# Kernel optimization log

Measured on AMD Instinct MI355X. Metric: run time of the kernel, lower is better.

Reference implementation:

```python
import jax, jax.numpy as jnp
import numpy as np

B, N_IN, N_OUT = 4096, 64, 64
M = N_IN * N_OUT


def setup_inputs() -> dict:
    key = jax.random.key(0)
    k1, k2, k3, k4 = jax.random.split(key, 4)
    I = jax.random.normal(k1, (B, N_IN, 4, 4), dtype=jnp.float32)
    # params: (rand - 0.5) * 1, matching torch init
    aW = (jax.random.uniform(k2, (M, 1, 1), dtype=jnp.float32) - 0.5)
    uW = (jax.random.uniform(k3, (M, 1, 3), dtype=jnp.float32) - 0.5)
    tW = (jax.random.uniform(k4, (M, 1, 3), dtype=jnp.float32) - 0.5)
    return {"I": I, "aW": aW, "uW": uW, "tW": tW}


def _build_WM(aW, uW, tW, n_in, n_out):
    m = aW.shape[0]
    a = aW.reshape(m, 1, 1)                       # angle per transform
    u = jax.nn.sigmoid(uW.reshape(m, 3))
    u = u / jnp.linalg.norm(u, axis=1, keepdims=True)  # unit axis
    ux, uy, uz = u[:, 0], u[:, 1], u[:, 2]
    z = jnp.zeros_like(ux)
    # skew-symmetric cross-product matrix K
    K = jnp.stack([z, -uz, uy,
                   uz, z, -ux,
                   -uy, ux, z], axis=1).reshape(m, 3, 3)
    uuT = u[:, :, None] * u[:, None, :]
    I3 = jnp.eye(3, dtype=aW.dtype)
    # Rodrigues: R = sin(a) K + cos(a)(I - uu^T) + uu^T
    rot = jnp.sin(a) * K + jnp.cos(a) * (I3 - uuT) + uuT
    top = jnp.concatenate([rot, tW.reshape(m, 3, 1)], axis=2)   # [m,3,4]
    bot = jnp.broadcast_to(jnp.array([[0.0, 0.0, 0.0, 1.0]], dtype=aW.dtype), (m, 1, 4))
    WM = jnp.concatenate([top, bot], axis=1)                    # [m,4,4]
    return WM.reshape(n_in, n_out, 4, 4)


def reference(I, aW, uW, tW):
    batch, n_in = I.shape[0], I.shape[1]
    n_out = aW.shape[0] // n_in
    WM = _build_WM(aW, uW, tW, n_in, n_out)       # [n_in, n_out, 4, 4] (batch-invariant)
    # A[b,j,k] = I[b,j] @ WM[j,k]
    A = jnp.einsum('bjxy,jkyz->jbkxz', I, WM)     # [n_in, B, n_out, 4, 4]
    init = jnp.broadcast_to(jnp.eye(4, dtype=I.dtype), (batch, n_out, 4, 4))
    def step(carry, Aj):
        return jnp.einsum('bkxy,bkyz->bkxz', carry, Aj), None
    O, _ = jax.lax.scan(step, init, A)            # sequential product over n_in
    return O                                      # [B, n_out, 4, 4]
```

## Files before the change

### kernel.cpp

```cpp
#include <hip/hip_runtime.h>

#define BATCH 4096
#define NIN   64
#define NOUT  64
#define M_TOT (NIN * NOUT)

__global__ __launch_bounds__(256) void build_wm_kernel(
    const float* __restrict__ aW, const float* __restrict__ uW,
    const float* __restrict__ tW, float4* __restrict__ WT) {
  int m = blockIdx.x * 256 + threadIdx.x;
  if (m >= M_TOT) return;
  int j = m >> 6, k = m & 63;

  float a  = aW[m];
  float ux = 1.f / (1.f + expf(-uW[3 * m + 0]));
  float uy = 1.f / (1.f + expf(-uW[3 * m + 1]));
  float uz = 1.f / (1.f + expf(-uW[3 * m + 2]));
  float inv = 1.f / sqrtf(ux * ux + uy * uy + uz * uz);
  ux *= inv; uy *= inv; uz *= inv;

  float sa = sinf(a), ca = cosf(a);
  float xx = ux * ux, yy = uy * uy, zz = uz * uz;
  float xy = ux * uy, xz = ux * uz, yz = uy * uz;

  float R00 = ca * (1.f - xx) + xx;
  float R01 = -sa * uz + ca * (-xy) + xy;
  float R02 =  sa * uy + ca * (-xz) + xz;
  float R10 =  sa * uz + ca * (-xy) + xy;
  float R11 = ca * (1.f - yy) + yy;
  float R12 = -sa * ux + ca * (-yz) + yz;
  float R20 = -sa * uy + ca * (-xz) + xz;
  float R21 =  sa * ux + ca * (-yz) + yz;
  float R22 = ca * (1.f - zz) + zz;

  float t0 = tW[3 * m + 0], t1 = tW[3 * m + 1], t2 = tW[3 * m + 2];

  WT[(j * 3 + 0) * 64 + k] = make_float4(R00, R01, R02, t0);
  WT[(j * 3 + 1) * 64 + k] = make_float4(R10, R11, R12, t1);
  WT[(j * 3 + 2) * 64 + k] = make_float4(R20, R21, R22, t2);
}


#define IMUL_TO(D0, D1, D2, D3, r, W0, W1, W2)                       \
  D0 = r.x * W0.x + r.y * W1.x + r.z * W2.x;                         \
  D1 = r.x * W0.y + r.y * W1.y + r.z * W2.y;                         \
  D2 = r.x * W0.z + r.y * W1.z + r.z * W2.z;                         \
  D3 = r.x * W0.w + r.y * W1.w + r.z * W2.w + r.w;

#define CMUL_ROW(x)                                                            \
  {                                                                            \
    float t0 = c[x*4+0]*A00 + c[x*4+1]*A10 + c[x*4+2]*A20 + c[x*4+3]*A30;      \
    float t1 = c[x*4+0]*A01 + c[x*4+1]*A11 + c[x*4+2]*A21 + c[x*4+3]*A31;      \
    float t2 = c[x*4+0]*A02 + c[x*4+1]*A12 + c[x*4+2]*A22 + c[x*4+3]*A32;      \
    float t3 = c[x*4+0]*A03 + c[x*4+1]*A13 + c[x*4+2]*A23 + c[x*4+3]*A33;      \
    c[x*4+0] = t0; c[x*4+1] = t1; c[x*4+2] = t2; c[x*4+3] = t3;                \
  }

__global__ __launch_bounds__(128) void chain_kernel(
    const float4* __restrict__ I4, const float4* __restrict__ WT,
    float4* __restrict__ O4) {
  const int t    = threadIdx.x;
  const int lane = t & 63;
  const int half = t >> 6;
  const int b    = (int)blockIdx.x;

  __shared__ float4 ILDS[256];
  __shared__ float  P[64][17];

  const float4* __restrict__ Isrc = I4 + (size_t)b * (NIN * 4);
  ILDS[t]       = Isrc[t];
  ILDS[t + 128] = Isrc[t + 128];
  __syncthreads();

  const float4* __restrict__ Wb = WT + (size_t)(half * 32 * 3) * 64 + lane;
  const int ibase = half * 128;

  float c[16];
  {
    float4 w0 = Wb[0], w1 = Wb[64], w2 = Wb[128];
    float4 r0 = ILDS[ibase + 0], r1 = ILDS[ibase + 1];
    float4 r2 = ILDS[ibase + 2], r3 = ILDS[ibase + 3];
    IMUL_TO(c[0],  c[1],  c[2],  c[3],  r0, w0, w1, w2)
    IMUL_TO(c[4],  c[5],  c[6],  c[7],  r1, w0, w1, w2)
    IMUL_TO(c[8],  c[9],  c[10], c[11], r2, w0, w1, w2)
    IMUL_TO(c[12], c[13], c[14], c[15], r3, w0, w1, w2)
  }

#pragma unroll 4
  for (int j = 1; j < 32; ++j) {
    float4 w0 = Wb[j * 192], w1 = Wb[j * 192 + 64], w2 = Wb[j * 192 + 128];
    float4 r0 = ILDS[ibase + j * 4 + 0], r1 = ILDS[ibase + j * 4 + 1];
    float4 r2 = ILDS[ibase + j * 4 + 2], r3 = ILDS[ibase + j * 4 + 3];
    float A00, A01, A02, A03, A10, A11, A12, A13;
    float A20, A21, A22, A23, A30, A31, A32, A33;
    IMUL_TO(A00, A01, A02, A03, r0, w0, w1, w2)
    IMUL_TO(A10, A11, A12, A13, r1, w0, w1, w2)
    IMUL_TO(A20, A21, A22, A23, r2, w0, w1, w2)
    IMUL_TO(A30, A31, A32, A33, r3, w0, w1, w2)
    CMUL_ROW(0) CMUL_ROW(1) CMUL_ROW(2) CMUL_ROW(3)
  }

  if (half == 1) {
#pragma unroll
    for (int i = 0; i < 16; i++) P[lane][i] = c[i];
  }
  __syncthreads();
  if (half == 0) {
    float A00 = P[lane][0],  A01 = P[lane][1];
    float A02 = P[lane][2],  A03 = P[lane][3];
    float A10 = P[lane][4],  A11 = P[lane][5];
    float A12 = P[lane][6],  A13 = P[lane][7];
    float A20 = P[lane][8],  A21 = P[lane][9];
    float A22 = P[lane][10], A23 = P[lane][11];
    float A30 = P[lane][12], A31 = P[lane][13];
    float A32 = P[lane][14], A33 = P[lane][15];

    CMUL_ROW(0)
    CMUL_ROW(1)
    CMUL_ROW(2)
    CMUL_ROW(3)

    float4* o = O4 + ((size_t)b * NOUT + lane) * 4;
    o[0] = make_float4(c[0],  c[1],  c[2],  c[3]);
    o[1] = make_float4(c[4],  c[5],  c[6],  c[7]);
    o[2] = make_float4(c[8],  c[9],  c[10], c[11]);
    o[3] = make_float4(c[12], c[13], c[14], c[15]);
  }
}

extern "C" void kernel_launch(void* const* d_in, const int* in_sizes, int n_in,
                              void* d_out, int out_size, void* d_ws, size_t ws_size,
                              hipStream_t stream) {
  const float* I  = (const float*)d_in[0];
  const float* aW = (const float*)d_in[1];
  const float* uW = (const float*)d_in[2];
  const float* tW = (const float*)d_in[3];

  float4* WT = (float4*)d_ws;

  build_wm_kernel<<<M_TOT / 256, 256, 0, stream>>>(aW, uW, tW, WT);
  chain_kernel<<<BATCH, 128, 0, stream>>>((const float4*)I, WT, (float4*)d_out);
}
```

Before: 67.10 us.

## Share staged weights across four batches per block with double-buffered LDS

Each 256-thread block now handles four batch elements, one wavefront each, and runs the full 64-step chain per wave instead of splitting it across two halves and merging through LDS. The weight matrices are staged cooperatively into a double-buffered LDS tile in chunks of four steps, with the next chunk prefetched into registers. This lets four batches share each weight load from global memory. The input rows are now read straight from global memory with a wave-uniform offset rather than staged in LDS. In exchange it adds a block barrier per chunk, doubles the serial chain length per wave, and removes the two-way split parallelism.

```diff
diff --git a/kernel.cpp b/kernel.cpp
--- a/kernel.cpp
+++ b/kernel.cpp
@@ -41,12 +41,6 @@
 }
 
 
-#define IMUL_TO(D0, D1, D2, D3, r, W0, W1, W2)                       \
-  D0 = r.x * W0.x + r.y * W1.x + r.z * W2.x;                         \
-  D1 = r.x * W0.y + r.y * W1.y + r.z * W2.y;                         \
-  D2 = r.x * W0.z + r.y * W1.z + r.z * W2.z;                         \
-  D3 = r.x * W0.w + r.y * W1.w + r.z * W2.w + r.w;
-
 #define CMUL_ROW(x)                                                            \
   {                                                                            \
     float t0 = c[x*4+0]*A00 + c[x*4+1]*A10 + c[x*4+2]*A20 + c[x*4+3]*A30;      \
@@ -56,76 +50,81 @@
     c[x*4+0] = t0; c[x*4+1] = t1; c[x*4+2] = t2; c[x*4+3] = t3;                \
   }
 
-__global__ __launch_bounds__(128) void chain_kernel(
+__global__ __launch_bounds__(256) void chain_kernel(
     const float4* __restrict__ I4, const float4* __restrict__ WT,
     float4* __restrict__ O4) {
   const int t    = threadIdx.x;
   const int lane = t & 63;
-  const int half = t >> 6;
-  const int b    = (int)blockIdx.x;
+  const int wid  = t >> 6;
+  const int b    = (int)blockIdx.x * 4 + wid;
 
-  __shared__ float4 ILDS[256];
-  __shared__ float  P[64][17];
+  __shared__ float4 buf[2][768];
 
-  const float4* __restrict__ Isrc = I4 + (size_t)b * (NIN * 4);
-  ILDS[t]       = Isrc[t];
-  ILDS[t + 128] = Isrc[t + 128];
+  const int ioff = __builtin_amdgcn_readfirstlane(b * (NIN * 4));
+  const float4* __restrict__ Ib = I4 + ioff;
+
+  float4 s0, s1, s2;
+
+  s0 = WT[t]; s1 = WT[t + 256]; s2 = WT[t + 512];
+  buf[0][t] = s0; buf[0][t + 256] = s1; buf[0][t + 512] = s2;
+  {
+    const float4* src = WT + 768;
+    s0 = src[t]; s1 = src[t + 256]; s2 = src[t + 512];
+  }
   __syncthreads();
 
-  const float4* __restrict__ Wb = WT + (size_t)(half * 32 * 3) * 64 + lane;
-  const int ibase = half * 128;
+  float c[16];
+#pragma unroll
+  for (int i = 0; i < 16; i++) c[i] = (i == 0 || i == 5 || i == 10 || i == 15) ? 1.f : 0.f;
 
-  float c[16];
-  {
-    float4 w0 = Wb[0], w1 = Wb[64], w2 = Wb[128];
-    float4 r0 = ILDS[ibase + 0], r1 = ILDS[ibase + 1];
-    float4 r2 = ILDS[ibase + 2], r3 = ILDS[ibase + 3];
-    IMUL_TO(c[0],  c[1],  c[2],  c[3],  r0, w0, w1, w2)
-    IMUL_TO(c[4],  c[5],  c[6],  c[7],  r1, w0, w1, w2)
-    IMUL_TO(c[8],  c[9],  c[10], c[11], r2, w0, w1, w2)
-    IMUL_TO(c[12], c[13], c[14], c[15], r3, w0, w1, w2)
+  for (int ch = 0; ch < 16; ++ch) {
+    const int slot = ch & 1;
+
+    if (ch < 15) {
+      buf[slot ^ 1][t] = s0;
+      buf[slot ^ 1][t + 256] = s1;
+      buf[slot ^ 1][t + 512] = s2;
+      if (ch < 14) {
+        const float4* src = WT + (size_t)(ch + 2) * 768;
+        s0 = src[t]; s1 = src[t + 256]; s2 = src[t + 512];
+      }
+    }
+
+#pragma unroll
+    for (int jj = 0; jj < 4; ++jj) {
+      const float4* wrow = &buf[slot][jj * 192];
+      float4 w0 = wrow[lane], w1 = wrow[64 + lane], w2 = wrow[128 + lane];
+      const int j = ch * 4 + jj;
+      float4 r0 = Ib[j * 4 + 0], r1 = Ib[j * 4 + 1];
+      float4 r2 = Ib[j * 4 + 2], r3 = Ib[j * 4 + 3];
+
+      float A00 = r0.x*w0.x + r0.y*w1.x + r0.z*w2.x;
+      float A01 = r0.x*w0.y + r0.y*w1.y + r0.z*w2.y;
+      float A02 = r0.x*w0.z + r0.y*w1.z + r0.z*w2.z;
+      float A03 = r0.x*w0.w + r0.y*w1.w + r0.z*w2.w + r0.w;
+      float A10 = r1.x*w0.x + r1.y*w1.x + r1.z*w2.x;
+      float A11 = r1.x*w0.y + r1.y*w1.y + r1.z*w2.y;
+      float A12 = r1.x*w0.z + r1.y*w1.z + r1.z*w2.z;
+      float A13 = r1.x*w0.w + r1.y*w1.w + r1.z*w2.w + r1.w;
+      float A20 = r2.x*w0.x + r2.y*w1.x + r2.z*w2.x;
+      float A21 = r2.x*w0.y + r2.y*w1.y + r2.z*w2.y;
+      float A22 = r2.x*w0.z + r2.y*w1.z + r2.z*w2.z;
+      float A23 = r2.x*w0.w + r2.y*w1.w + r2.z*w2.w + r2.w;
+      float A30 = r3.x*w0.x + r3.y*w1.x + r3.z*w2.x;
+      float A31 = r3.x*w0.y + r3.y*w1.y + r3.z*w2.y;
+      float A32 = r3.x*w0.z + r3.y*w1.z + r3.z*w2.z;
+      float A33 = r3.x*w0.w + r3.y*w1.w + r3.z*w2.w + r3.w;
+
+      CMUL_ROW(0) CMUL_ROW(1) CMUL_ROW(2) CMUL_ROW(3)
+    }
+    __syncthreads();
   }
 
-#pragma unroll 4
-  for (int j = 1; j < 32; ++j) {
-    float4 w0 = Wb[j * 192], w1 = Wb[j * 192 + 64], w2 = Wb[j * 192 + 128];
-    float4 r0 = ILDS[ibase + j * 4 + 0], r1 = ILDS[ibase + j * 4 + 1];
-    float4 r2 = ILDS[ibase + j * 4 + 2], r3 = ILDS[ibase + j * 4 + 3];
-    float A00, A01, A02, A03, A10, A11, A12, A13;
-    float A20, A21, A22, A23, A30, A31, A32, A33;
-    IMUL_TO(A00, A01, A02, A03, r0, w0, w1, w2)
-    IMUL_TO(A10, A11, A12, A13, r1, w0, w1, w2)
-    IMUL_TO(A20, A21, A22, A23, r2, w0, w1, w2)
-    IMUL_TO(A30, A31, A32, A33, r3, w0, w1, w2)
-    CMUL_ROW(0) CMUL_ROW(1) CMUL_ROW(2) CMUL_ROW(3)
-  }
-
-  if (half == 1) {
-#pragma unroll
-    for (int i = 0; i < 16; i++) P[lane][i] = c[i];
-  }
-  __syncthreads();
-  if (half == 0) {
-    float A00 = P[lane][0],  A01 = P[lane][1];
-    float A02 = P[lane][2],  A03 = P[lane][3];
-    float A10 = P[lane][4],  A11 = P[lane][5];
-    float A12 = P[lane][6],  A13 = P[lane][7];
-    float A20 = P[lane][8],  A21 = P[lane][9];
-    float A22 = P[lane][10], A23 = P[lane][11];
-    float A30 = P[lane][12], A31 = P[lane][13];
-    float A32 = P[lane][14], A33 = P[lane][15];
-
-    CMUL_ROW(0)
-    CMUL_ROW(1)
-    CMUL_ROW(2)
-    CMUL_ROW(3)
-
-    float4* o = O4 + ((size_t)b * NOUT + lane) * 4;
-    o[0] = make_float4(c[0],  c[1],  c[2],  c[3]);
-    o[1] = make_float4(c[4],  c[5],  c[6],  c[7]);
-    o[2] = make_float4(c[8],  c[9],  c[10], c[11]);
-    o[3] = make_float4(c[12], c[13], c[14], c[15]);
-  }
+  float4* o = O4 + ((size_t)b * NOUT + lane) * 4;
+  o[0] = make_float4(c[0],  c[1],  c[2],  c[3]);
+  o[1] = make_float4(c[4],  c[5],  c[6],  c[7]);
+  o[2] = make_float4(c[8],  c[9],  c[10], c[11]);
+  o[3] = make_float4(c[12], c[13], c[14], c[15]);
 }
 
 extern "C" void kernel_launch(void* const* d_in, const int* in_sizes, int n_in,
@@ -139,5 +138,5 @@
   float4* WT = (float4*)d_ws;
 
   build_wm_kernel<<<M_TOT / 256, 256, 0, stream>>>(aW, uW, tW, WT);
-  chain_kernel<<<BATCH, 128, 0, stream>>>((const float4*)I, WT, (float4*)d_out);
+  chain_kernel<<<BATCH / 4, 256, 0, stream>>>((const float4*)I, WT, (float4*)d_out);
 }
```

Result: slower. 81.26 us (+21.1%).
